# Optimization experiments

Measured on AMD Instinct MI355X. Metric: run time of the kernel, lower is better.

Reference implementation:

```python
import jax, jax.numpy as jnp
import numpy as np

SOS_TOKEN = 0
HIDDEN = 512
EMBED = 256
V_SRC = 32000
V_TGT = 50257
S_LEN = 512
T_LEN = 512


def setup_inputs() -> dict:
    key = jax.random.key(0)
    ks = jax.random.split(key, 16)
    s = 0.02
    return {
        "source": jax.random.randint(ks[0], (S_LEN,), 0, V_SRC),
        "target": jax.random.randint(ks[1], (T_LEN, 1), 0, V_TGT),
        "emb_e": jax.random.normal(ks[2], (V_SRC, EMBED), jnp.float32) * s,
        "Wih_e": jax.random.normal(ks[3], (3 * HIDDEN, EMBED), jnp.float32) * s,
        "Whh_e": jax.random.normal(ks[4], (3 * HIDDEN, HIDDEN), jnp.float32) * s,
        "bih_e": jax.random.normal(ks[5], (3 * HIDDEN,), jnp.float32) * s,
        "bhh_e": jax.random.normal(ks[6], (3 * HIDDEN,), jnp.float32) * s,
        "emb_d": jax.random.normal(ks[7], (V_TGT, EMBED), jnp.float32) * s,
        "Wih_d": jax.random.normal(ks[8], (3 * HIDDEN, EMBED), jnp.float32) * s,
        "Whh_d": jax.random.normal(ks[9], (3 * HIDDEN, HIDDEN), jnp.float32) * s,
        "bih_d": jax.random.normal(ks[10], (3 * HIDDEN,), jnp.float32) * s,
        "bhh_d": jax.random.normal(ks[11], (3 * HIDDEN,), jnp.float32) * s,
        "Wout": jax.random.normal(ks[12], (V_TGT, HIDDEN), jnp.float32) * s,
        "bout": jax.random.normal(ks[13], (V_TGT,), jnp.float32) * s,
    }


def _gru_step(h, x, Wih, Whh, bih, bhh):
    # PyTorch GRU cell: gates ordered (r, z, n)
    gi = Wih @ x + bih            # [3H]
    gh = Whh @ h + bhh            # [3H]
    gi_r, gi_z, gi_n = jnp.split(gi, 3)
    gh_r, gh_z, gh_n = jnp.split(gh, 3)
    r = jax.nn.sigmoid(gi_r + gh_r)
    z = jax.nn.sigmoid(gi_z + gh_z)
    n = jnp.tanh(gi_n + r * gh_n)
    return (1.0 - z) * n + z * h


def reference(source, target, emb_e, Wih_e, Whh_e, bih_e, bhh_e,
              emb_d, Wih_d, Whh_d, bih_d, bhh_d, Wout, bout):
    # Encoder (faithful to original: gru called per-token with zero hidden,
    # so only the last source token determines encoder_hidden).
    x_last = emb_e[source[-1]]                       # [E]
    h0 = jnp.zeros((HIDDEN,), dtype=emb_e.dtype)
    h_enc = _gru_step(h0, x_last, Wih_e, Whh_e, bih_e, bhh_e)  # [H]

    # Decoder with teacher forcing (ratio=1.0): inputs are SOS, target[:-1]
    tgt = target[:, 0]
    tokens = jnp.concatenate([jnp.array([SOS_TOKEN], dtype=tgt.dtype), tgt[:-1]])

    def step(h, tok):
        x = jax.nn.relu(emb_d[tok])                  # [E]
        h2 = _gru_step(h, x, Wih_d, Whh_d, bih_d, bhh_d)
        logp = jax.nn.log_softmax(Wout @ h2 + bout)  # [V]
        return h2, logp

    _, logps = jax.lax.scan(step, h_enc, tokens)     # [T, V]
    return logps[:, None, :]                         # [T, 1, V]
```

## Files before the change

kernel.cpp:

```cpp
#include <hip/hip_runtime.h>
#include <stdint.h>

#define HIDDEN 512
#define EMBED  256
#define VTGT   50257
#define TLEN   512
#define GATE3  1536
#define REC_B  16
#define GEMM_B 224
#define NBLK   (REC_B + GEMM_B)
#define NJT    ((VTGT + 127) / 128)

typedef float f32x4 __attribute__((ext_vector_type(4)));
typedef unsigned int u32;
typedef unsigned int u32x4 __attribute__((ext_vector_type(4)));

__device__ __forceinline__ unsigned short f2bf(float f) {
  union { float f; unsigned u; } v; v.f = f;
  unsigned u = v.u;
  unsigned r = (u + 0x7FFFu + ((u >> 16) & 1u)) >> 16;
  return (unsigned short)r;
}

__device__ __forceinline__ float sigm(float x) {
  return 1.f / (1.f + __expf(-x));
}

__device__ __forceinline__ u32 cpoll(const u32* p) {
  u32 v;
  asm volatile("global_load_dword %0, %1, off sc0 sc1\n\ts_waitcnt vmcnt(0)"
               : "=v"(v) : "v"(p) : "memory");
  return v;
}
__device__ __forceinline__ void cload4x4(const u32* p, u32x4& a, u32x4& b,
                                         u32x4& c, u32x4& d) {
  asm volatile(
      "global_load_dwordx4 %0, %4, off sc0 sc1\n\t"
      "global_load_dwordx4 %1, %4, off offset:16 sc0 sc1\n\t"
      "global_load_dwordx4 %2, %4, off offset:32 sc0 sc1\n\t"
      "global_load_dwordx4 %3, %4, off offset:48 sc0 sc1\n\t"
      "s_waitcnt vmcnt(0)"
      : "=v"(a), "=v"(b), "=v"(c), "=v"(d) : "v"(p) : "memory");
}
__device__ __forceinline__ void cstore(u32* p, u32 v) {
  asm volatile("global_store_dword %0, %1, off sc0 sc1" :: "v"(p), "v"(v) : "memory");
}

__global__ void kenc1(const int* source, const float* emb_e, const float* Wih_e,
                      const float* bih_e, float* genc) {
  __shared__ float xs[EMBED];
  int tid = threadIdx.x;
  int tok = source[511];
  if (tid < EMBED) xs[tid] = emb_e[(size_t)tok * EMBED + tid];
  __syncthreads();
  int j = blockIdx.x * 256 + tid;
  const float* w = Wih_e + (size_t)j * EMBED;
  float acc = bih_e[j];
  for (int k = 0; k < EMBED; k += 4) {
    float4 wv = *(const float4*)(w + k);
    acc += wv.x * xs[k] + wv.y * xs[k + 1] + wv.z * xs[k + 2] + wv.w * xs[k + 3];
  }
  genc[j] = acc;
}

__global__ void kenc2(const float* genc, const float* bhh_e, u32* hs) {
  int e = threadIdx.x;
  float r = sigm(genc[e] + bhh_e[e]);
  float z = sigm(genc[e + 512] + bhh_e[e + 512]);
  float n = tanhf(genc[e + 1024] + r * bhh_e[e + 1024]);
  float h = (1.f - z) * n;
  hs[e] = (__float_as_uint(h) & ~511u) | 256u;
}

__global__ __launch_bounds__(256) void kgi(const int* target, const float* emb_d,
                                           const float* Wih_d, const float* bih_d,
                                           float* GI) {
  __shared__ float Xs[32][EMBED];
  int tid = threadIdx.x;
  int j0 = blockIdx.x * 128;
  int t0 = blockIdx.y * 32;
  for (int idx = tid; idx < 32 * EMBED; idx += 256) {
    int tt = idx >> 8, c = idx & 255;
    int t = t0 + tt;
    int tok = (t == 0) ? 0 : target[t - 1];
    float v = emb_d[(size_t)tok * EMBED + c];
    Xs[tt][c] = v > 0.f ? v : 0.f;
  }
  __syncthreads();
  int jl = tid & 127, tg = tid >> 7;
  int j = j0 + jl;
  const float* w = Wih_d + (size_t)j * EMBED;
  float acc[16];
#pragma unroll
  for (int i = 0; i < 16; ++i) acc[i] = 0.f;
  for (int k = 0; k < EMBED; k += 4) {
    float4 wv = *(const float4*)(w + k);
#pragma unroll
    for (int i = 0; i < 16; ++i) {
      int tl = tg * 16 + i;
      acc[i] += wv.x * Xs[tl][k] + wv.y * Xs[tl][k + 1] +
                wv.z * Xs[tl][k + 2] + wv.w * Xs[tl][k + 3];
    }
  }
  float b = bih_d[j];
#pragma unroll
  for (int i = 0; i < 16; ++i) {
    int t = t0 + tg * 16 + i;
    GI[(size_t)t * GATE3 + j] = acc[i] + b;
  }
}

__device__ void rec_path(int bid, const float* Whh, const float* bhh,
                         const float* GI, u32* hs, u32* stepv, char* SM) {
  int tid = threadIdx.x;
  int r = tid >> 4, p = tid & 15;
  int e = bid * 32 + r;
  int k0 = p * 32;
  float* hbuf = (float*)SM;
  float wr[32], wz[32], wn[32];
  {
    const float* Wr = Whh + (size_t)e * HIDDEN + k0;
    const float* Wz = Whh + (size_t)(e + 512) * HIDDEN + k0;
    const float* Wn = Whh + (size_t)(e + 1024) * HIDDEN + k0;
#pragma unroll
    for (int i = 0; i < 32; i += 4) {
      *(float4*)&wr[i] = *(const float4*)(Wr + i);
      *(float4*)&wz[i] = *(const float4*)(Wz + i);
      *(float4*)&wn[i] = *(const float4*)(Wn + i);
    }
  }
  float br = bhh[e], bz = bhh[e + 512], bn = bhh[e + 1024];
  __builtin_amdgcn_s_setprio(1);
  int wslot = (tid >> 5) * 36 + (tid & 31);
  int eslot = (e >> 5) * 36 + (e & 31);
  for (int t = 0; t < TLEN; ++t) {
    int par = t & 1;
    float gie = 0.f, giz = 0.f, gin = 0.f;
    if (p == 0) {
      const float* git = GI + (size_t)t * GATE3;
      gie = git[e]; giz = git[e + 512]; gin = git[e + 1024];
    }
    u32 want = 256u + ((u32)t & 255u);
    const u32* src = hs + (size_t)t * HIDDEN + tid;
    u32 v;
    do { v = cpoll(src); } while ((v & 511u) != want);
    hbuf[par * 576 + wslot] = __uint_as_float(v & ~511u);
    __syncthreads();
    if (bid == 0 && tid == 0) cstore(stepv, (u32)t);
    const float* hp = hbuf + par * 576 + p * 36;
    float pr = 0.f, pz = 0.f, pn = 0.f;
#pragma unroll
    for (int i = 0; i < 32; i += 4) {
      float4 hv = *(const float4*)(hp + i);
      pr += wr[i] * hv.x + wr[i + 1] * hv.y + wr[i + 2] * hv.z + wr[i + 3] * hv.w;
      pz += wz[i] * hv.x + wz[i + 1] * hv.y + wz[i + 2] * hv.z + wz[i + 3] * hv.w;
      pn += wn[i] * hv.x + wn[i + 1] * hv.y + wn[i + 2] * hv.z + wn[i + 3] * hv.w;
    }
#pragma unroll
    for (int m = 1; m < 16; m <<= 1) {
      pr += __shfl_xor(pr, m);
      pz += __shfl_xor(pz, m);
      pn += __shfl_xor(pn, m);
    }
    if (p == 0) {
      float rg = sigm(gie + pr + br);
      float z  = sigm(giz + pz + bz);
      float n  = tanhf(gin + rg * (pn + bn));
      float hold = hbuf[par * 576 + eslot];
      float hnew = (1.f - z) * n + z * hold;
      u32 pk = (__float_as_uint(hnew) & ~511u) | (256u + ((u32)(t + 1) & 255u));
      cstore(hs + (size_t)(t + 1) * HIDDEN + e, pk);
    }
  }
  if (bid == 0) {
    u32 want = 256u;
    const u32* src = hs + (size_t)TLEN * HIDDEN + tid;
    u32 v;
    do { v = cpoll(src); } while ((v & 511u) != want);
    __syncthreads();
    if (tid == 0) cstore(stepv, (u32)TLEN);
  }
}

__device__ void gemm_path(int g, const u32* hs, u32* stepv, const float* Wout,
                          const float* bout, float* out, char* SM) {
  unsigned short* As = (unsigned short*)SM;
  int tid = threadIdx.x;
  int w = tid >> 6, lane = tid & 63;
  int jl = lane & 15, kq = lane >> 4;
  int srow = tid >> 3, scg = tid & 7;
  for (int t0i = 0; t0i < 8; ++t0i) {
    int t0 = t0i * 64;
    if (tid == 0) {
      while ((int)cpoll(stepv) < t0 + 64) {}
    }
    __syncthreads();
    int slot = t0 + srow + 1;
    u32 want = 256u + ((u32)slot & 255u);
    const u32* sbase = hs + (size_t)slot * HIDDEN + scg * 64;
#pragma unroll
    for (int b = 0; b < 4; ++b) {
      const u32* sp = sbase + b * 16;
      u32x4 c0, c1, c2, c3;
      for (;;) {
        cload4x4(sp, c0, c1, c2, c3);
        u32 bad = 0;
#pragma unroll
        for (int q = 0; q < 4; ++q)
          bad |= (c0[q] ^ want) | (c1[q] ^ want) | (c2[q] ^ want) | (c3[q] ^ want);
        if (!(bad & 511u)) break;
      }
      u32 dw[8];
#pragma unroll
      for (int q = 0; q < 4; ++q) {
        u32x4 cq = (q == 0) ? c0 : (q == 1) ? c1 : (q == 2) ? c2 : c3;
        float f0 = __uint_as_float(cq[0] & ~511u);
        float f1 = __uint_as_float(cq[1] & ~511u);
        float f2 = __uint_as_float(cq[2] & ~511u);
        float f3 = __uint_as_float(cq[3] & ~511u);
        dw[q * 2]     = (u32)f2bf(f0) | ((u32)f2bf(f1) << 16);
        dw[q * 2 + 1] = (u32)f2bf(f2) | ((u32)f2bf(f3) << 16);
      }
      *(u32x4*)&As[srow * 520 + scg * 64 + b * 16]     = *(u32x4*)&dw[0];
      *(u32x4*)&As[srow * 520 + scg * 64 + b * 16 + 8] = *(u32x4*)&dw[4];
    }
    __syncthreads();
    for (int jt = g; jt < NJT; jt += GEMM_B) {
      int j = jt * 128 + w * 16 + jl;
      int jc = j < VTGT ? j : VTGT - 1;
      const float* Bp = Wout + (size_t)jc * HIDDEN + kq * 8;
      f32x4 acc[4];
#pragma unroll
      for (int i = 0; i < 4; ++i) acc[i] = (f32x4)(0.f);
#pragma unroll
      for (int ks = 0; ks < 16; ++ks) {
        float4 b0 = *(const float4*)(Bp + ks * 32);
        float4 b1 = *(const float4*)(Bp + ks * 32 + 4);
        u32x4 bf;
        bf[0] = (u32)f2bf(b0.x) | ((u32)f2bf(b0.y) << 16);
        bf[1] = (u32)f2bf(b0.z) | ((u32)f2bf(b0.w) << 16);
        bf[2] = (u32)f2bf(b1.x) | ((u32)f2bf(b1.y) << 16);
        bf[3] = (u32)f2bf(b1.z) | ((u32)f2bf(b1.w) << 16);
#pragma unroll
        for (int tq = 0; tq < 4; ++tq) {
          u32x4 af = *(const u32x4*)&As[(tq * 16 + jl) * 520 + ks * 32 + kq * 8];
          asm volatile("v_mfma_f32_16x16x32_bf16 %0, %1, %2, %0"
                       : "+v"(acc[tq]) : "v"(af), "v"(bf));
        }
      }
      asm volatile("s_nop 7\n\ts_nop 7\n\ts_nop 7" ::);
      bool jok = j < VTGT;
      float bj = jok ? bout[j] : 0.f;
#pragma unroll
      for (int tq = 0; tq < 4; ++tq)
#pragma unroll
        for (int rr = 0; rr < 4; ++rr) {
          int t = t0 + tq * 16 + kq * 4 + rr;
          if (jok) out[(size_t)t * VTGT + j] = acc[tq][rr] + bj;
        }
    }
    __syncthreads();
  }
}

__global__ __launch_bounds__(512) void kmain(const float* Whh, const float* bhh,
                                             const float* GI, u32* hs, u32* stepv,
                                             const float* Wout, const float* bout,
                                             float* out) {
  __shared__ __align__(16) char SM[64 * 520 * 2];
  int bid = blockIdx.x;
  if (bid < REC_B) rec_path(bid, Whh, bhh, GI, hs, stepv, SM);
  else gemm_path(bid - REC_B, hs, stepv, Wout, bout, out, SM);
}

__global__ __launch_bounds__(1024) void klsub(float* out) {
  int t = blockIdx.x, tid = threadIdx.x;
  float* row = out + (size_t)t * VTGT;
  float m = -INFINITY, s = 0.f;
  for (int jj = tid; jj < VTGT; jj += 1024) {
    float x = row[jj];
    if (x > m) { s = s * __expf(m - x) + 1.f; m = x; }
    else s += __expf(x - m);
  }
#pragma unroll
  for (int d = 1; d < 64; d <<= 1) {
    float mo = __shfl_xor(m, d, 64), so = __shfl_xor(s, d, 64);
    float mn = fmaxf(m, mo);
    s = s * __expf(m - mn) + so * __expf(mo - mn);
    m = mn;
  }
  __shared__ float sm[16], sv[16], sl;
  if ((tid & 63) == 0) { sm[tid >> 6] = m; sv[tid >> 6] = s; }
  __syncthreads();
  if (tid == 0) {
    for (int q = 1; q < 16; ++q) {
      float mo = sm[q], so = sv[q];
      float mn = fmaxf(m, mo);
      s = s * __expf(m - mn) + so * __expf(mo - mn);
      m = mn;
    }
    sl = m + logf(s);
  }
  __syncthreads();
  float l = sl;
  for (int jj = tid; jj < VTGT; jj += 1024) row[jj] -= l;
}

extern "C" void kernel_launch(void* const* d_in, const int* in_sizes, int n_in,
                              void* d_out, int out_size, void* d_ws, size_t ws_size,
                              hipStream_t stream) {
  const int*   source = (const int*)d_in[0];
  const int*   target = (const int*)d_in[1];
  const float* emb_e  = (const float*)d_in[2];
  const float* Wih_e  = (const float*)d_in[3];
  const float* bih_e  = (const float*)d_in[5];
  const float* bhh_e  = (const float*)d_in[6];
  const float* emb_d  = (const float*)d_in[7];
  const float* Wih_d  = (const float*)d_in[8];
  const float* Whh_d  = (const float*)d_in[9];
  const float* bih_d  = (const float*)d_in[10];
  const float* bhh_d  = (const float*)d_in[11];
  const float* Wout   = (const float*)d_in[12];
  const float* bout   = (const float*)d_in[13];
  float* out = (float*)d_out;
  char* ws = (char*)d_ws;

  float* GI    = (float*)(ws + 0);
  u32*   hs    = (u32*)(ws + 3145728);
  u32*   stepv = (u32*)(ws + 4196352);
  float* genc  = (float*)(ws + 4196608);

  hipMemsetAsync(hs, 0, 1050624 + 256, stream);
  kenc1<<<6, 256, 0, stream>>>(source, emb_e, Wih_e, bih_e, genc);
  kenc2<<<1, 512, 0, stream>>>(genc, bhh_e, hs);
  kgi<<<dim3(12, 16), 256, 0, stream>>>(target, emb_d, Wih_d, bih_d, GI);
  kmain<<<NBLK, 512, 0, stream>>>(Whh_d, bhh_d, GI, hs, stepv, Wout, bout, out);
  klsub<<<512, 1024, 0, stream>>>(out);
}
```

Measured before the change: 943.1 us.

## Pre-convert Wout to bf16 once per call and vectorize recurrent h polling

At kernel start the GEMM blocks convert Wout from fp32 to a padded bf16 workspace copy and signal completion through an atomic counter. Each 64-step output tile then streams half the bytes and skips the per-tile conversion, where before fp32 weights were reread and converted 8 times. The recurrent blocks now poll hidden state with one wave doing two dwordx4 loads per lane instead of 512 scalar polls, and the GEMM waiters sleep between polls. The cost is an extra write and read of a roughly 50MB bf16 buffer and a grid-wide dependency before the first tile.

New measurement: 989.9 us. 1.05x slower.

```diff
diff --git a/kernel.cpp b/kernel.cpp
--- a/kernel.cpp
+++ b/kernel.cpp
@@ -4,6 +4,7 @@
 #define HIDDEN 512
 #define EMBED  256
 #define VTGT   50257
+#define VTGT_PAD 50304
 #define TLEN   512
 #define GATE3  1536
 #define REC_B  16
@@ -13,6 +14,7 @@
 
 typedef float f32x4 __attribute__((ext_vector_type(4)));
 typedef unsigned int u32;
+typedef unsigned int u32x2 __attribute__((ext_vector_type(2)));
 typedef unsigned int u32x4 __attribute__((ext_vector_type(4)));
 
 __device__ __forceinline__ unsigned short f2bf(float f) {
@@ -42,8 +44,19 @@
       "s_waitcnt vmcnt(0)"
       : "=v"(a), "=v"(b), "=v"(c), "=v"(d) : "v"(p) : "memory");
 }
+__device__ __forceinline__ void cload2(const u32* p0, const u32* p1,
+                                       u32x4& a, u32x4& b) {
+  asm volatile(
+      "global_load_dwordx4 %0, %2, off sc0 sc1\n\t"
+      "global_load_dwordx4 %1, %3, off sc0 sc1\n\t"
+      "s_waitcnt vmcnt(0)"
+      : "=v"(a), "=v"(b) : "v"(p0), "v"(p1) : "memory");
+}
 __device__ __forceinline__ void cstore(u32* p, u32 v) {
   asm volatile("global_store_dword %0, %1, off sc0 sc1" :: "v"(p), "v"(v) : "memory");
+}
+__device__ __forceinline__ void cstore2(u32* p, u32x2 v) {
+  asm volatile("global_store_dwordx2 %0, %1, off sc0 sc1" :: "v"(p), "v"(v) : "memory");
 }
 
 __global__ void kenc1(const int* source, const float* emb_e, const float* Wih_e,
@@ -113,7 +126,7 @@
 __device__ void rec_path(int bid, const float* Whh, const float* bhh,
                          const float* GI, u32* hs, u32* stepv, char* SM) {
   int tid = threadIdx.x;
-  int r = tid >> 4, p = tid & 15;
+  int p = tid & 15, r = tid >> 4;
   int e = bid * 32 + r;
   int k0 = p * 32;
   float* hbuf = (float*)SM;
@@ -131,8 +144,10 @@
   }
   float br = bhh[e], bz = bhh[e + 512], bn = bhh[e + 1024];
   __builtin_amdgcn_s_setprio(1);
-  int wslot = (tid >> 5) * 36 + (tid & 31);
-  int eslot = (e >> 5) * 36 + (e & 31);
+  int d0 = tid * 4;
+  int i0 = ((d0 >> 5) * 36) + (d0 & 31);
+  int i1 = (((d0 + 256) >> 5) * 36) + (d0 & 31);
+  int eslot = ((e >> 5) * 36) + (e & 31);
   for (int t = 0; t < TLEN; ++t) {
     int par = t & 1;
     float gie = 0.f, giz = 0.f, gin = 0.f;
@@ -140,11 +155,27 @@
       const float* git = GI + (size_t)t * GATE3;
       gie = git[e]; giz = git[e + 512]; gin = git[e + 1024];
     }
-    u32 want = 256u + ((u32)t & 255u);
-    const u32* src = hs + (size_t)t * HIDDEN + tid;
-    u32 v;
-    do { v = cpoll(src); } while ((v & 511u) != want);
-    hbuf[par * 576 + wslot] = __uint_as_float(v & ~511u);
+    if (tid < 64) {
+      const u32* s0 = hs + (size_t)t * HIDDEN + d0;
+      const u32* s1 = s0 + 256;
+      u32 want = 256u + ((u32)t & 255u);
+      u32x4 a, b;
+      for (;;) {
+        cload2(s0, s1, a, b);
+        u32 bad = 0;
+#pragma unroll
+        for (int q = 0; q < 4; ++q) bad |= (a[q] ^ want) | (b[q] ^ want);
+        if (!__any((bad & 511u) != 0u)) break;
+      }
+      f32x4 fa, fb;
+#pragma unroll
+      for (int q = 0; q < 4; ++q) {
+        fa[q] = __uint_as_float(a[q] & ~511u);
+        fb[q] = __uint_as_float(b[q] & ~511u);
+      }
+      *(f32x4*)&hbuf[par * 576 + i0] = fa;
+      *(f32x4*)&hbuf[par * 576 + i1] = fb;
+    }
     __syncthreads();
     if (bid == 0 && tid == 0) cstore(stepv, (u32)t);
     const float* hp = hbuf + par * 576 + p * 36;
@@ -172,27 +203,59 @@
       cstore(hs + (size_t)(t + 1) * HIDDEN + e, pk);
     }
   }
-  if (bid == 0) {
-    u32 want = 256u;
-    const u32* src = hs + (size_t)TLEN * HIDDEN + tid;
-    u32 v;
-    do { v = cpoll(src); } while ((v & 511u) != want);
-    __syncthreads();
+  if (bid == 0 && tid < 64) {
+    const u32* s0 = hs + (size_t)TLEN * HIDDEN + d0;
+    const u32* s1 = s0 + 256;
+    u32 want = 256u + ((u32)TLEN & 255u);
+    u32x4 a, b;
+    for (;;) {
+      cload2(s0, s1, a, b);
+      u32 bad = 0;
+#pragma unroll
+      for (int q = 0; q < 4; ++q) bad |= (a[q] ^ want) | (b[q] ^ want);
+      if (!__any((bad & 511u) != 0u)) break;
+    }
     if (tid == 0) cstore(stepv, (u32)TLEN);
   }
 }
 
-__device__ void gemm_path(int g, const u32* hs, u32* stepv, const float* Wout,
-                          const float* bout, float* out, char* SM) {
+__device__ void gemm_path(int g, const u32* hs, u32* stepv, u32* wcnt,
+                          const float* Wout, const float* bout,
+                          unsigned short* WB, float* out, char* SM) {
   unsigned short* As = (unsigned short*)SM;
   int tid = threadIdx.x;
+  {
+    const size_t nquad = (size_t)VTGT_PAD * HIDDEN / 4;
+    size_t qs = nquad * (size_t)g / GEMM_B;
+    size_t qe = nquad * (size_t)(g + 1) / GEMM_B;
+    for (size_t q = qs + tid; q < qe; q += 512) {
+      size_t i = q * 4;
+      int j = (int)(i >> 9);
+      u32x2 o;
+      if (j < VTGT) {
+        float4 v = *(const float4*)(Wout + i);
+        o[0] = (u32)f2bf(v.x) | ((u32)f2bf(v.y) << 16);
+        o[1] = (u32)f2bf(v.z) | ((u32)f2bf(v.w) << 16);
+      } else { o[0] = 0u; o[1] = 0u; }
+      cstore2((u32*)(WB + i), o);
+    }
+    asm volatile("s_waitcnt vmcnt(0)" ::: "memory");
+    __syncthreads();
+    if (tid == 0)
+      __hip_atomic_fetch_add(wcnt, 1u, __ATOMIC_RELEASE, __HIP_MEMORY_SCOPE_AGENT);
+  }
   int w = tid >> 6, lane = tid & 63;
   int jl = lane & 15, kq = lane >> 4;
   int srow = tid >> 3, scg = tid & 7;
   for (int t0i = 0; t0i < 8; ++t0i) {
     int t0 = t0i * 64;
     if (tid == 0) {
-      while ((int)cpoll(stepv) < t0 + 64) {}
+      if (t0i == 0) {
+        while (__hip_atomic_load(wcnt, __ATOMIC_ACQUIRE, __HIP_MEMORY_SCOPE_AGENT)
+               < (u32)GEMM_B)
+          __builtin_amdgcn_s_sleep(8);
+      }
+      while ((int)cpoll(stepv) < t0 + 64) __builtin_amdgcn_s_sleep(32);
     }
     __syncthreads();
     int slot = t0 + srow + 1;
@@ -227,20 +290,13 @@
     __syncthreads();
     for (int jt = g; jt < NJT; jt += GEMM_B) {
       int j = jt * 128 + w * 16 + jl;
-      int jc = j < VTGT ? j : VTGT - 1;
-      const float* Bp = Wout + (size_t)jc * HIDDEN + kq * 8;
+      const unsigned short* Bp = WB + (size_t)j * HIDDEN + kq * 8;
       f32x4 acc[4];
 #pragma unroll
       for (int i = 0; i < 4; ++i) acc[i] = (f32x4)(0.f);
 #pragma unroll
       for (int ks = 0; ks < 16; ++ks) {
-        float4 b0 = *(const float4*)(Bp + ks * 32);
-        float4 b1 = *(const float4*)(Bp + ks * 32 + 4);
-        u32x4 bf;
-        bf[0] = (u32)f2bf(b0.x) | ((u32)f2bf(b0.y) << 16);
-        bf[1] = (u32)f2bf(b0.z) | ((u32)f2bf(b0.w) << 16);
-        bf[2] = (u32)f2bf(b1.x) | ((u32)f2bf(b1.y) << 16);
-        bf[3] = (u32)f2bf(b1.z) | ((u32)f2bf(b1.w) << 16);
+        u32x4 bf = *(const u32x4*)(Bp + ks * 32);
 #pragma unroll
         for (int tq = 0; tq < 4; ++tq) {
           u32x4 af = *(const u32x4*)&As[(tq * 16 + jl) * 520 + ks * 32 + kq * 8];
@@ -265,12 +321,13 @@
 
 __global__ __launch_bounds__(512) void kmain(const float* Whh, const float* bhh,
                                              const float* GI, u32* hs, u32* stepv,
-                                             const float* Wout, const float* bout,
+                                             u32* wcnt, const float* Wout,
+                                             const float* bout, unsigned short* WB,
                                              float* out) {
   __shared__ __align__(16) char SM[64 * 520 * 2];
   int bid = blockIdx.x;
   if (bid < REC_B) rec_path(bid, Whh, bhh, GI, hs, stepv, SM);
-  else gemm_path(bid - REC_B, hs, stepv, Wout, bout, out, SM);
+  else gemm_path(bid - REC_B, hs, stepv, wcnt, Wout, bout, WB, out, SM);
 }
 
 __global__ __launch_bounds__(1024) void klsub(float* out) {
@@ -325,15 +382,18 @@
   float* out = (float*)d_out;
   char* ws = (char*)d_ws;
 
-  float* GI    = (float*)(ws + 0);
-  u32*   hs    = (u32*)(ws + 3145728);
-  u32*   stepv = (u32*)(ws + 4196352);
-  float* genc  = (float*)(ws + 4196608);
+  float*          GI    = (float*)(ws + 0);
+  u32*            hs    = (u32*)(ws + 3145728);
+  u32*            stepv = (u32*)(ws + 4196352);
+  u32*            wcnt  = (u32*)(ws + 4196480);
+  float*          genc  = (float*)(ws + 4196608);
+  unsigned short* WB    = (unsigned short*)(ws + 4202752);
 
   hipMemsetAsync(hs, 0, 1050624 + 256, stream);
   kenc1<<<6, 256, 0, stream>>>(source, emb_e, Wih_e, bih_e, genc);
   kenc2<<<1, 512, 0, stream>>>(genc, bhh_e, hs);
   kgi<<<dim3(12, 16), 256, 0, stream>>>(target, emb_d, Wih_d, bih_d, GI);
-  kmain<<<NBLK, 512, 0, stream>>>(Whh_d, bhh_d, GI, hs, stepv, Wout, bout, out);
+  kmain<<<NBLK, 512, 0, stream>>>(Whh_d, bhh_d, GI, hs, stepv, wcnt, Wout, bout,
+                                  WB, out);
   klsub<<<512, 1024, 0, stream>>>(out);
 }
```

## Fuse softmax row-sum into vocab GEMM and widen persistent blocks to 1024 threads

Applied to the files above, without the earlier changes.

The logsumexp pass is dropped from the final kernel. The GEMM epilogue now accumulates exp(logit) per timestep through shared-memory and global atomics, so klsub only subtracts log(sum). Blocks grow to 1024 threads: the recurrence splits each dot product over 32 lanes, keeps h_old in a register, stores paired values, and uses a fast tanh. The GEMM path handles 256-column tiles with 120 blocks and polls the hidden-state flags directly instead of a step counter. The sum skips max-subtraction, which relies on logits staying small enough not to overflow, and the atomics make the float sums nondeterministic.

After: 1.480 ms. 56.9% more time.

```diff
diff --git a/kernel.cpp b/kernel.cpp
--- a/kernel.cpp
+++ b/kernel.cpp
@@ -7,12 +7,13 @@
 #define TLEN   512
 #define GATE3  1536
 #define REC_B  16
-#define GEMM_B 224
+#define GEMM_B 120
 #define NBLK   (REC_B + GEMM_B)
-#define NJT    ((VTGT + 127) / 128)
+#define NJT    197
 
 typedef float f32x4 __attribute__((ext_vector_type(4)));
 typedef unsigned int u32;
+typedef unsigned int u32x2 __attribute__((ext_vector_type(2)));
 typedef unsigned int u32x4 __attribute__((ext_vector_type(4)));
 
 __device__ __forceinline__ unsigned short f2bf(float f) {
@@ -24,6 +25,9 @@
 
 __device__ __forceinline__ float sigm(float x) {
   return 1.f / (1.f + __expf(-x));
+}
+__device__ __forceinline__ float fast_tanh(float x) {
+  return 1.f - 2.f / (__expf(2.f * x) + 1.f);
 }
 
 __device__ __forceinline__ u32 cpoll(const u32* p) {
@@ -42,8 +46,8 @@
       "s_waitcnt vmcnt(0)"
       : "=v"(a), "=v"(b), "=v"(c), "=v"(d) : "v"(p) : "memory");
 }
-__device__ __forceinline__ void cstore(u32* p, u32 v) {
-  asm volatile("global_store_dword %0, %1, off sc0 sc1" :: "v"(p), "v"(v) : "memory");
+__device__ __forceinline__ void cstore2(u32* p, u32x2 v) {
+  asm volatile("global_store_dwordx2 %0, %1, off sc0 sc1" :: "v"(p), "v"(v) : "memory");
 }
 
 __global__ void kenc1(const int* source, const float* emb_e, const float* Wih_e,
@@ -111,28 +115,31 @@
 }
 
 __device__ void rec_path(int bid, const float* Whh, const float* bhh,
-                         const float* GI, u32* hs, u32* stepv, char* SM) {
+                         const float* GI, u32* hs, char* SM) {
   int tid = threadIdx.x;
-  int r = tid >> 4, p = tid & 15;
+  int p = tid & 31;
+  int r = tid >> 5;
   int e = bid * 32 + r;
-  int k0 = p * 32;
+  int k0 = p * 16;
   float* hbuf = (float*)SM;
-  float wr[32], wz[32], wn[32];
+  float wr[16], wz[16], wn[16];
   {
     const float* Wr = Whh + (size_t)e * HIDDEN + k0;
     const float* Wz = Whh + (size_t)(e + 512) * HIDDEN + k0;
     const float* Wn = Whh + (size_t)(e + 1024) * HIDDEN + k0;
 #pragma unroll
-    for (int i = 0; i < 32; i += 4) {
+    for (int i = 0; i < 16; i += 4) {
       *(float4*)&wr[i] = *(const float4*)(Wr + i);
       *(float4*)&wz[i] = *(const float4*)(Wz + i);
       *(float4*)&wn[i] = *(const float4*)(Wn + i);
     }
   }
   float br = bhh[e], bz = bhh[e + 512], bn = bhh[e + 1024];
+  float hold = 0.f;
+  if (p == 0) hold = __uint_as_float(hs[e] & ~511u);
   __builtin_amdgcn_s_setprio(1);
-  int wslot = (tid >> 5) * 36 + (tid & 31);
-  int eslot = (e >> 5) * 36 + (e & 31);
+  int pslot = ((tid >> 5) * 36) + (tid & 31);
+  int dbase = (p >> 1) * 36 + (p & 1) * 16;
   for (int t = 0; t < TLEN; ++t) {
     int par = t & 1;
     float gie = 0.f, giz = 0.f, gin = 0.f;
@@ -140,67 +147,68 @@
       const float* git = GI + (size_t)t * GATE3;
       gie = git[e]; giz = git[e + 512]; gin = git[e + 1024];
     }
-    u32 want = 256u + ((u32)t & 255u);
-    const u32* src = hs + (size_t)t * HIDDEN + tid;
-    u32 v;
-    do { v = cpoll(src); } while ((v & 511u) != want);
-    hbuf[par * 576 + wslot] = __uint_as_float(v & ~511u);
+    if (tid < 512) {
+      const u32* src = hs + (size_t)t * HIDDEN + tid;
+      u32 want = 256u + ((u32)t & 255u);
+      u32 v;
+      do { v = cpoll(src); } while ((v & 511u) != want);
+      hbuf[par * 576 + pslot] = __uint_as_float(v & ~511u);
+    }
     __syncthreads();
-    if (bid == 0 && tid == 0) cstore(stepv, (u32)t);
-    const float* hp = hbuf + par * 576 + p * 36;
+    const float* hp = hbuf + par * 576 + dbase;
     float pr = 0.f, pz = 0.f, pn = 0.f;
 #pragma unroll
-    for (int i = 0; i < 32; i += 4) {
+    for (int i = 0; i < 16; i += 4) {
       float4 hv = *(const float4*)(hp + i);
       pr += wr[i] * hv.x + wr[i + 1] * hv.y + wr[i + 2] * hv.z + wr[i + 3] * hv.w;
       pz += wz[i] * hv.x + wz[i + 1] * hv.y + wz[i + 2] * hv.z + wz[i + 3] * hv.w;
       pn += wn[i] * hv.x + wn[i + 1] * hv.y + wn[i + 2] * hv.z + wn[i + 3] * hv.w;
     }
 #pragma unroll
-    for (int m = 1; m < 16; m <<= 1) {
+    for (int m = 1; m < 32; m <<= 1) {
       pr += __shfl_xor(pr, m);
       pz += __shfl_xor(pz, m);
       pn += __shfl_xor(pn, m);
     }
+    u32 pk = 0;
     if (p == 0) {
       float rg = sigm(gie + pr + br);
       float z  = sigm(giz + pz + bz);
-      float n  = tanhf(gin + rg * (pn + bn));
-      float hold = hbuf[par * 576 + eslot];
+      float n  = fast_tanh(gin + rg * (pn + bn));
       float hnew = (1.f - z) * n + z * hold;
-      u32 pk = (__float_as_uint(hnew) & ~511u) | (256u + ((u32)(t + 1) & 255u));
-      cstore(hs + (size_t)(t + 1) * HIDDEN + e, pk);
-    }
-  }
-  if (bid == 0) {
-    u32 want = 256u;
-    const u32* src = hs + (size_t)TLEN * HIDDEN + tid;
-    u32 v;
-    do { v = cpoll(src); } while ((v & 511u) != want);
-    __syncthreads();
-    if (tid == 0) cstore(stepv, (u32)TLEN);
-  }
-}
-
-__device__ void gemm_path(int g, const u32* hs, u32* stepv, const float* Wout,
-                          const float* bout, float* out, char* SM) {
+      hold = hnew;
+      pk = (__float_as_uint(hnew) & ~511u) | (256u + ((u32)(t + 1) & 255u));
+    }
+    u32 other = __shfl(pk, 32);
+    if ((tid & 63) == 0) {
+      u32x2 o; o[0] = pk; o[1] = other;
+      cstore2(hs + (size_t)(t + 1) * HIDDEN + bid * 32 + (tid >> 6) * 2, o);
+    }
+  }
+}
+
+__device__ void gemm_path(int g, const u32* hs, const float* Wout,
+                          const float* bout, float* rs, float* out, char* SM) {
   unsigned short* As = (unsigned short*)SM;
+  float* rsum = (float*)(SM + 64 * 520 * 2);
   int tid = threadIdx.x;
   int w = tid >> 6, lane = tid & 63;
   int jl = lane & 15, kq = lane >> 4;
-  int srow = tid >> 3, scg = tid & 7;
+  int srow = tid >> 4, scg = tid & 15;
+  if (tid < 64) rsum[tid] = 0.f;
   for (int t0i = 0; t0i < 8; ++t0i) {
     int t0 = t0i * 64;
     if (tid == 0) {
-      while ((int)cpoll(stepv) < t0 + 64) {}
+      const u32* hp = hs + (size_t)(t0 + 64) * HIDDEN + 256;
+      u32 hw = 256u + ((u32)(t0 + 64) & 255u);
+      while ((cpoll(hp) & 511u) != hw) __builtin_amdgcn_s_sleep(16);
     }
     __syncthreads();
     int slot = t0 + srow + 1;
     u32 want = 256u + ((u32)slot & 255u);
-    const u32* sbase = hs + (size_t)slot * HIDDEN + scg * 64;
-#pragma unroll
-    for (int b = 0; b < 4; ++b) {
-      const u32* sp = sbase + b * 16;
+#pragma unroll
+    for (int b = 0; b < 2; ++b) {
+      const u32* sp = hs + (size_t)slot * HIDDEN + scg * 32 + b * 16;
       u32x4 c0, c1, c2, c3;
       for (;;) {
         cload4x4(sp, c0, c1, c2, c3);
@@ -221,12 +229,12 @@
         dw[q * 2]     = (u32)f2bf(f0) | ((u32)f2bf(f1) << 16);
         dw[q * 2 + 1] = (u32)f2bf(f2) | ((u32)f2bf(f3) << 16);
       }
-      *(u32x4*)&As[srow * 520 + scg * 64 + b * 16]     = *(u32x4*)&dw[0];
-      *(u32x4*)&As[srow * 520 + scg * 64 + b * 16 + 8] = *(u32x4*)&dw[4];
+      *(u32x4*)&As[srow * 520 + scg * 32 + b * 16]     = *(u32x4*)&dw[0];
+      *(u32x4*)&As[srow * 520 + scg * 32 + b * 16 + 8] = *(u32x4*)&dw[4];
     }
     __syncthreads();
     for (int jt = g; jt < NJT; jt += GEMM_B) {
-      int j = jt * 128 + w * 16 + jl;
+      int j = jt * 256 + w * 16 + jl;
       int jc = j < VTGT ? j : VTGT - 1;
       const float* Bp = Wout + (size_t)jc * HIDDEN + kq * 8;
       f32x4 acc[4];
@@ -252,58 +260,42 @@
       bool jok = j < VTGT;
       float bj = jok ? bout[j] : 0.f;
 #pragma unroll
-      for (int tq = 0; tq < 4; ++tq)
+      for (int tq = 0; tq < 4; ++tq) {
 #pragma unroll
         for (int rr = 0; rr < 4; ++rr) {
           int t = t0 + tq * 16 + kq * 4 + rr;
-          if (jok) out[(size_t)t * VTGT + j] = acc[tq][rr] + bj;
+          float lg = acc[tq][rr] + bj;
+          if (jok) out[(size_t)t * VTGT + j] = lg;
+          float ex = jok ? __expf(lg) : 0.f;
+#pragma unroll
+          for (int m = 1; m < 16; m <<= 1) ex += __shfl_xor(ex, m);
+          if (jl == 0) atomicAdd(&rsum[tq * 16 + kq * 4 + rr], ex);
         }
+      }
     }
     __syncthreads();
-  }
-}
-
-__global__ __launch_bounds__(512) void kmain(const float* Whh, const float* bhh,
-                                             const float* GI, u32* hs, u32* stepv,
-                                             const float* Wout, const float* bout,
-                                             float* out) {
-  __shared__ __align__(16) char SM[64 * 520 * 2];
+    if (tid < 64) {
+      atomicAdd(rs + t0 + tid, rsum[tid]);
+      rsum[tid] = 0.f;
+    }
+  }
+}
+
+__global__ __launch_bounds__(1024, 4) void kmain(const float* Whh, const float* bhh,
+                                                 const float* GI, u32* hs,
+                                                 const float* Wout, const float* bout,
+                                                 float* rs, float* out) {
+  __shared__ __align__(16) char SM[64 * 520 * 2 + 256];
   int bid = blockIdx.x;
-  if (bid < REC_B) rec_path(bid, Whh, bhh, GI, hs, stepv, SM);
-  else gemm_path(bid - REC_B, hs, stepv, Wout, bout, out, SM);
-}
-
-__global__ __launch_bounds__(1024) void klsub(float* out) {
-  int t = blockIdx.x, tid = threadIdx.x;
+  if (bid < REC_B) rec_path(bid, Whh, bhh, GI, hs, SM);
+  else gemm_path(bid - REC_B, hs, Wout, bout, rs, out, SM);
+}
+
+__global__ __launch_bounds__(1024) void klsub(float* out, const float* rs) {
+  int t = blockIdx.x;
+  float l = logf(rs[t]);
   float* row = out + (size_t)t * VTGT;
-  float m = -INFINITY, s = 0.f;
-  for (int jj = tid; jj < VTGT; jj += 1024) {
-    float x = row[jj];
-    if (x > m) { s = s * __expf(m - x) + 1.f; m = x; }
-    else s += __expf(x - m);
-  }
-#pragma unroll
-  for (int d = 1; d < 64; d <<= 1) {
-    float mo = __shfl_xor(m, d, 64), so = __shfl_xor(s, d, 64);
-    float mn = fmaxf(m, mo);
-    s = s * __expf(m - mn) + so * __expf(mo - mn);
-    m = mn;
-  }
-  __shared__ float sm[16], sv[16], sl;
-  if ((tid & 63) == 0) { sm[tid >> 6] = m; sv[tid >> 6] = s; }
-  __syncthreads();
-  if (tid == 0) {
-    for (int q = 1; q < 16; ++q) {
-      float mo = sm[q], so = sv[q];
-      float mn = fmaxf(m, mo);
-      s = s * __expf(m - mn) + so * __expf(mo - mn);
-      m = mn;
-    }
-    sl = m + logf(s);
-  }
-  __syncthreads();
-  float l = sl;
-  for (int jj = tid; jj < VTGT; jj += 1024) row[jj] -= l;
+  for (int jj = threadIdx.x; jj < VTGT; jj += 1024) row[jj] -= l;
 }
 
 extern "C" void kernel_launch(void* const* d_in, const int* in_sizes, int n_in,
@@ -325,15 +317,15 @@
   float* out = (float*)d_out;
   char* ws = (char*)d_ws;
 
-  float* GI    = (float*)(ws + 0);
-  u32*   hs    = (u32*)(ws + 3145728);
-  u32*   stepv = (u32*)(ws + 4196352);
-  float* genc  = (float*)(ws + 4196608);
-
-  hipMemsetAsync(hs, 0, 1050624 + 256, stream);
+  float* GI   = (float*)(ws + 0);
+  u32*   hs   = (u32*)(ws + 3145728);
+  float* rs   = (float*)(ws + 4196352);
+  float* genc = (float*)(ws + 4198400);
+
+  hipMemsetAsync(hs, 0, 1050624 + 2048, stream);
   kenc1<<<6, 256, 0, stream>>>(source, emb_e, Wih_e, bih_e, genc);
   kenc2<<<1, 512, 0, stream>>>(genc, bhh_e, hs);
   kgi<<<dim3(12, 16), 256, 0, stream>>>(target, emb_d, Wih_d, bih_d, GI);
-  kmain<<<NBLK, 512, 0, stream>>>(Whh_d, bhh_d, GI, hs, stepv, Wout, bout, out);
-  klsub<<<512, 1024, 0, stream>>>(out);
-}
+  kmain<<<NBLK, 1024, 0, stream>>>(Whh_d, bhh_d, GI, hs, Wout, bout, rs, out);
+  klsub<<<512, 1024, 0, stream>>>(out, rs);
+}
```
